# Kernel optimization log

Hardware: AMD Instinct MI355X
Metric: run time of the kernel (lower is better)

The kernel has to match this reference:

```python
import jax, jax.numpy as jnp
import numpy as np

EMBED_DIM = 1024
NUM_HEADS = 16
HEAD_DIM = EMBED_DIM // NUM_HEADS
CHUNK_SIZE = 10
LEFT_CONTEXT = 25
RIGHT_CONTEXT = 0
NEG_INF = -1e30  # stands in for float('-inf') additive mask, safe under softmax


def chunk_attention_mask(seq_len: int) -> jnp.ndarray:
    """Vectorized version of the per-row Python loop mask builder.
    Row i may attend to: its own chunk [chunk_start, chunk_end), the left
    context [i-left_context, chunk_start), and the right context
    [chunk_end, i+right_context+1)."""
    i = jnp.arange(seq_len)[:, None]
    j = jnp.arange(seq_len)[None, :]
    chunk_start = (i // CHUNK_SIZE) * CHUNK_SIZE
    chunk_end = jnp.minimum(chunk_start + CHUNK_SIZE, seq_len)
    in_chunk = (j >= chunk_start) & (j < chunk_end)
    in_left = (j >= i - LEFT_CONTEXT) & (j < chunk_start)
    in_right = (j >= chunk_end) & (j < jnp.minimum(seq_len, i + RIGHT_CONTEXT + 1))
    allowed = in_chunk | in_left | in_right
    return jnp.where(allowed, 0.0, NEG_INF).astype(jnp.float32)


def setup_inputs() -> dict:
    key = jax.random.key(0)
    ks = jax.random.split(key, 9)
    B, S, E = 2, 2048, EMBED_DIM
    s = 1.0 / np.sqrt(E)
    return {
        "hidden_states": jax.random.normal(ks[0], (B, S, E), jnp.float32),
        "Wq": jax.random.normal(ks[1], (E, E), jnp.float32) * s,
        "bq": jax.random.normal(ks[2], (E,), jnp.float32) * 0.02,
        "Wk": jax.random.normal(ks[3], (E, E), jnp.float32) * s,
        "bk": jax.random.normal(ks[4], (E,), jnp.float32) * 0.02,
        "Wv": jax.random.normal(ks[5], (E, E), jnp.float32) * s,
        "bv": jax.random.normal(ks[6], (E,), jnp.float32) * 0.02,
        "Wo": jax.random.normal(ks[7], (E, E), jnp.float32) * s,
        "bo": jax.random.normal(ks[8], (E,), jnp.float32) * 0.02,
    }


def reference(hidden_states, Wq, bq, Wk, bk, Wv, bv, Wo, bo):
    B, S, E = hidden_states.shape
    H, D = NUM_HEADS, HEAD_DIM
    scaling = D ** -0.5

    def proj(x, W, b):  # nn.Linear: x @ W.T + b, then split heads -> [B,H,S,D]
        y = jnp.einsum('bse,fe->bsf', x, W) + b
        return y.reshape(B, S, H, D).transpose(0, 2, 1, 3)

    q = proj(hidden_states, Wq, bq) * scaling
    k = proj(hidden_states, Wk, bk)
    v = proj(hidden_states, Wv, bv)

    scores = jnp.einsum('bhsd,bhtd->bhst', q, k)  # [B,H,S,S]
    scores = scores + chunk_attention_mask(S)[None, None]
    probs = jax.nn.softmax(scores, axis=-1)
    out = jnp.einsum('bhst,bhtd->bhsd', probs, v)  # [B,H,S,D]
    out = out.transpose(0, 2, 1, 3).reshape(B, S, E)
    out = jnp.einsum('bse,fe->bsf', out, Wo) + bo
    return out
```

## Files before the change

kernel.cpp:

```cpp
#include <hip/hip_runtime.h>
#include <stdint.h>

typedef unsigned short u16;
typedef __attribute__((ext_vector_type(8))) short short8;
typedef __attribute__((ext_vector_type(4))) short short4v;
typedef __attribute__((ext_vector_type(4))) float f32x4;

#define AS1 __attribute__((address_space(1)))
#define AS3 __attribute__((address_space(3)))

__device__ __forceinline__ u16 f2bf(float f) {
  uint32_t x = __builtin_bit_cast(uint32_t, f);
  uint32_t r = (x + 0x7fffu + ((x >> 16) & 1u)) >> 16;
  return (u16)r;
}
__device__ __forceinline__ float bf2f(u16 u) {
  return __builtin_bit_cast(float, (uint32_t)u << 16);
}

__device__ __forceinline__ void conv8(const float* __restrict__ s, u16* __restrict__ d, float sc) {
  float4 a = *(const float4*)s;
  float4 b = *(const float4*)(s + 4);
  union { u16 u[8]; uint4 v; } pk;
  pk.u[0] = f2bf(a.x * sc); pk.u[1] = f2bf(a.y * sc); pk.u[2] = f2bf(a.z * sc); pk.u[3] = f2bf(a.w * sc);
  pk.u[4] = f2bf(b.x * sc); pk.u[5] = f2bf(b.y * sc); pk.u[6] = f2bf(b.z * sc); pk.u[7] = f2bf(b.w * sc);
  *(uint4*)d = pk.v;
}
__device__ __forceinline__ void copy8f(const float* __restrict__ s, float* __restrict__ d, float sc) {
  float4 a = *(const float4*)s;
  float4 b = *(const float4*)(s + 4);
  a.x *= sc; a.y *= sc; a.z *= sc; a.w *= sc;
  b.x *= sc; b.y *= sc; b.z *= sc; b.w *= sc;
  *(float4*)d = a; *(float4*)(d + 4) = b;
}

__global__ void pack_kernel(const float* __restrict__ X,
                            const float* __restrict__ Wq, const float* __restrict__ bq,
                            const float* __restrict__ Wk, const float* __restrict__ bk,
                            const float* __restrict__ Wv, const float* __restrict__ bv,
                            const float* __restrict__ Wo,
                            u16* __restrict__ Xbf, u16* __restrict__ Wcat,
                            u16* __restrict__ Wobf, float* __restrict__ bcat) {
  int t = blockIdx.x * blockDim.x + threadIdx.x;
  if (t < 524288) { conv8(X + (size_t)t * 8, Xbf + (size_t)t * 8, 1.f); return; }
  t -= 524288;
  if (t < 131072) { conv8(Wq + (size_t)t * 8, Wcat + (size_t)t * 8, 0.125f); return; }
  t -= 131072;
  if (t < 131072) { conv8(Wk + (size_t)t * 8, Wcat + 1048576 + (size_t)t * 8, 1.f); return; }
  t -= 131072;
  if (t < 131072) { conv8(Wv + (size_t)t * 8, Wcat + 2097152 + (size_t)t * 8, 1.f); return; }
  t -= 131072;
  if (t < 131072) { conv8(Wo + (size_t)t * 8, Wobf + (size_t)t * 8, 1.f); return; }
  t -= 131072;
  if (t < 128) { copy8f(bq + t * 8, bcat + t * 8, 0.125f); return; }
  t -= 128;
  if (t < 128) { copy8f(bk + t * 8, bcat + 1024 + t * 8, 1.f); return; }
  t -= 128;
  if (t < 128) { copy8f(bv + t * 8, bcat + 2048 + t * 8, 1.f); return; }
}

template <int BN, bool OUT_BF16>
__global__ __launch_bounds__(256)
void gemm_bt(const u16* __restrict__ A, const u16* __restrict__ Bt,
             const float* __restrict__ bias, u16* __restrict__ Cbf,
             float* __restrict__ Cf, int M, int N, int K) {
  constexpr int SEG_A = 8;
  constexpr int SEG_B = BN / 16;
  constexpr int NSEG = SEG_A + SEG_B;
  constexpr int NI = BN / 32;
  __shared__ u16 As[2][128 * 32];
  __shared__ u16 Bs[2][BN * 32];
  const int wv = threadIdx.x >> 6;
  const int lane = threadIdx.x & 63;
  const int bm = blockIdx.x, bn = blockIdx.y;
  const int wm = wv >> 1, wn = wv & 1;
  const int lrow = lane & 15, quad = lane >> 4;

  f32x4 acc[4][NI];
#pragma unroll
  for (int i = 0; i < 4; ++i)
#pragma unroll
    for (int j = 0; j < NI; ++j) acc[i][j] = (f32x4){0.f, 0.f, 0.f, 0.f};

  const long arow = (long)bm * 128;
  const long brow = (long)bn * BN;
  const int srow = lane >> 2;
  const int scol = ((lane & 3) ^ ((lane >> 3) & 3)) * 8;
  const int swz = (quad ^ ((lrow >> 1) & 3)) * 8;

  auto stage = [&](int nb, int k0) {
#pragma unroll
    for (int it = 0; it < NSEG / 4; ++it) {
      const int s = wv * (NSEG / 4) + it;
      const u16* g;
      u16* l;
      if (s < SEG_A) {
        g = A + (arow + s * 16 + srow) * K + k0 + scol;
        l = (u16*)As[nb] + s * 512;
      } else {
        g = Bt + (brow + (s - SEG_A) * 16 + srow) * K + k0 + scol;
        l = (u16*)Bs[nb] + (s - SEG_A) * 512;
      }
      __builtin_amdgcn_global_load_lds((AS1 void*)g, (AS3 void*)l, 16, 0, 0);
    }
  };

  stage(0, 0);
  int cur = 0;
  for (int k0 = 0; k0 < K; k0 += 32) {
    __syncthreads();
    if (k0 + 32 < K) stage(cur ^ 1, k0 + 32);

    short8 af[4], bfr[NI];
#pragma unroll
    for (int mi = 0; mi < 4; ++mi)
      af[mi] = *(const short8*)(As[cur] + (wm * 64 + mi * 16 + lrow) * 32 + swz);
#pragma unroll
    for (int ni = 0; ni < NI; ++ni)
      bfr[ni] = *(const short8*)(Bs[cur] + (wn * (BN / 2) + ni * 16 + lrow) * 32 + swz);
#pragma unroll
    for (int mi = 0; mi < 4; ++mi)
#pragma unroll
      for (int ni = 0; ni < NI; ++ni)
        acc[mi][ni] = __builtin_amdgcn_mfma_f32_16x16x32_bf16(af[mi], bfr[ni], acc[mi][ni], 0, 0, 0);
    cur ^= 1;
  }

#pragma unroll
  for (int mi = 0; mi < 4; ++mi) {
#pragma unroll
    for (int ni = 0; ni < NI; ++ni) {
      const int col = bn * BN + wn * (BN / 2) + ni * 16 + lrow;
      const float bv = bias[col];
#pragma unroll
      for (int r = 0; r < 4; ++r) {
        const int row = bm * 128 + wm * 64 + mi * 16 + quad * 4 + r;
        const float v = acc[mi][ni][r] + bv;
        if constexpr (OUT_BF16) Cbf[(long)row * N + col] = f2bf(v);
        else Cf[(long)row * N + col] = v;
      }
    }
  }
}

#define NCH 205
#define VT_STRIDE 68
#define PB_STRIDE 72
#define WAVE_LDS (64 * VT_STRIDE + 16 * PB_STRIDE)

__global__ __launch_bounds__(256)
void attn_kernel(const u16* __restrict__ QKV, u16* __restrict__ ctx) {
  __shared__ __align__(16) u16 lds[4 * WAVE_LDS];
  const int wv = threadIdx.x >> 6;
  const int lane = threadIdx.x & 63;
  u16* Vt = lds + wv * WAVE_LDS;
  u16* Pb = Vt + 64 * VT_STRIDE;

  const int n = lane & 15, quad = lane >> 4;

  const int gw = blockIdx.x * 4 + wv;
  const int b = gw / (16 * NCH);
  int rem = gw - b * 16 * NCH;
  const int h = rem / NCH;
  const int c = rem - h * NCH;
  const int cs = c * 10;
  const int nq = min(10, 2048 - cs);
  const int w0 = max(cs - 25, 0);
  const int L = cs + nq - w0;

  const long base = ((long)b * 2048) * 3072 + (long)h * 64;

  for (int idx = lane; idx < (64 * VT_STRIDE) / 8; idx += 64)
    *(uint4*)(Vt + idx * 8) = (uint4){0, 0, 0, 0};
  for (int idx = lane; idx < (16 * PB_STRIDE) / 8; idx += 64)
    *(uint4*)(Pb + idx * 8) = (uint4){0, 0, 0, 0};

  for (int j = 0; j < L; ++j)
    Vt[lane * VT_STRIDE + j] = QKV[base + (long)(w0 + j) * 3072 + 2048 + lane];

  const int mclamp = min(n, nq - 1);
  const long qrow = base + (long)(cs + mclamp) * 3072;
  short8 aq0 = *(const short8*)(QKV + qrow + quad * 8);
  short8 aq1 = *(const short8*)(QKV + qrow + 32 + quad * 8);

  f32x4 sc[3];
#pragma unroll
  for (int t = 0; t < 3; ++t) {
    const int jj = min(16 * t + n, L - 1);
    const long krow = base + (long)(w0 + jj) * 3072 + 1024;
    short8 bk0 = *(const short8*)(QKV + krow + quad * 8);
    short8 bk1 = *(const short8*)(QKV + krow + 32 + quad * 8);
    f32x4 z = (f32x4){0.f, 0.f, 0.f, 0.f};
    z = __builtin_amdgcn_mfma_f32_16x16x32_bf16(aq0, bk0, z, 0, 0, 0);
    sc[t] = __builtin_amdgcn_mfma_f32_16x16x32_bf16(aq1, bk1, z, 0, 0, 0);
  }

#pragma unroll
  for (int r = 0; r < 4; ++r) {
    const int i = cs + quad * 4 + r;
    const int jlo = max(i - 25, 0) - w0;
    float v0 = (n >= jlo && n < L)      ? sc[0][r] : -1e30f;
    float v1 = (16 + n >= jlo && 16 + n < L) ? sc[1][r] : -1e30f;
    float v2 = (32 + n >= jlo && 32 + n < L) ? sc[2][r] : -1e30f;
    float m = fmaxf(v0, fmaxf(v1, v2));
#pragma unroll
    for (int off = 8; off > 0; off >>= 1) m = fmaxf(m, __shfl_xor(m, off));
    float p0 = __expf(v0 - m), p1 = __expf(v1 - m), p2 = __expf(v2 - m);
    float sum = p0 + p1 + p2;
#pragma unroll
    for (int off = 8; off > 0; off >>= 1) sum += __shfl_xor(sum, off);
    const float inv = 1.f / sum;
    u16* prow = Pb + (quad * 4 + r) * PB_STRIDE;
    prow[n]      = f2bf(p0 * inv);
    prow[16 + n] = f2bf(p1 * inv);
    prow[32 + n] = f2bf(p2 * inv);
  }

  short8 ap0 = *(const short8*)(Pb + n * PB_STRIDE + quad * 8);
  short8 ap1 = *(const short8*)(Pb + n * PB_STRIDE + 32 + quad * 8);
  f32x4 o[4];
#pragma unroll
  for (int dt = 0; dt < 4; ++dt) {
    const u16* vrow = Vt + (dt * 16 + n) * VT_STRIDE;
    short4v l0 = *(const short4v*)(vrow + quad * 8);
    short4v h0 = *(const short4v*)(vrow + quad * 8 + 4);
    short4v l1 = *(const short4v*)(vrow + 32 + quad * 8);
    short4v h1 = *(const short4v*)(vrow + 32 + quad * 8 + 4);
    short8 bv0 = __builtin_shufflevector(l0, h0, 0, 1, 2, 3, 4, 5, 6, 7);
    short8 bv1 = __builtin_shufflevector(l1, h1, 0, 1, 2, 3, 4, 5, 6, 7);
    f32x4 z = (f32x4){0.f, 0.f, 0.f, 0.f};
    z = __builtin_amdgcn_mfma_f32_16x16x32_bf16(ap0, bv0, z, 0, 0, 0);
    o[dt] = __builtin_amdgcn_mfma_f32_16x16x32_bf16(ap1, bv1, z, 0, 0, 0);
  }

#pragma unroll
  for (int dt = 0; dt < 4; ++dt) {
#pragma unroll
    for (int r = 0; r < 4; ++r) {
      const int row = quad * 4 + r;
      if (row < nq)
        ctx[((long)b * 2048 + cs + row) * 1024 + h * 64 + dt * 16 + n] = f2bf(o[dt][r]);
    }
  }
}

extern "C" void kernel_launch(void* const* d_in, const int* in_sizes, int n_in,
                              void* d_out, int out_size, void* d_ws, size_t ws_size,
                              hipStream_t stream) {
  const float* X  = (const float*)d_in[0];
  const float* Wq = (const float*)d_in[1];
  const float* bq = (const float*)d_in[2];
  const float* Wk = (const float*)d_in[3];
  const float* bk = (const float*)d_in[4];
  const float* Wv = (const float*)d_in[5];
  const float* bv = (const float*)d_in[6];
  const float* Wo = (const float*)d_in[7];
  const float* bo = (const float*)d_in[8];
  float* out = (float*)d_out;

  char* ws = (char*)d_ws;
  u16* Xbf   = (u16*)(ws);
  u16* Wcat  = (u16*)(ws + 8388608);
  u16* Wobf  = (u16*)(ws + 14680064);
  float* bcat = (float*)(ws + 16777216);
  u16* QKV   = (u16*)(ws + 16789504);
  u16* ctx   = (u16*)(ws + 41955328);

  pack_kernel<<<4098, 256, 0, stream>>>(X, Wq, bq, Wk, bk, Wv, bv, Wo, Xbf, Wcat, Wobf, bcat);
  gemm_bt<128, true ><<<dim3(32, 24), 256, 0, stream>>>(Xbf, Wcat, bcat, QKV, nullptr, 4096, 3072, 1024);
  attn_kernel<<<1640, 256, 0, stream>>>(QKV, ctx);
  gemm_bt<64, false><<<dim3(32, 16), 256, 0, stream>>>(ctx, Wobf, bo, nullptr, out, 4096, 1024, 1024);
}
```

Measured before the change: 163.0 us.

## Triple-buffer GEMM LDS stages with explicit vmcnt waits for deeper prefetch

Changes the bf16 GEMM mainloop from double to triple buffering in LDS, issuing global-to-LDS loads two k-steps ahead. Manual s_waitcnt vmcnt counts replace the implicit full wait, so a single barrier per iteration only waits for the oldest stage. The aim is to hide more global load latency. In exchange it uses more LDS per block, which may lower occupancy, and the hand-tuned vmcnt values depend on the per-wave load count.

```diff
diff --git a/kernel.cpp b/kernel.cpp
--- a/kernel.cpp
+++ b/kernel.cpp
@@ -67,9 +67,10 @@
   constexpr int SEG_A = 8;
   constexpr int SEG_B = BN / 16;
   constexpr int NSEG = SEG_A + SEG_B;
+  constexpr int LPW = NSEG / 4;
   constexpr int NI = BN / 32;
-  __shared__ u16 As[2][128 * 32];
-  __shared__ u16 Bs[2][BN * 32];
+  __shared__ u16 As[3][128 * 32];
+  __shared__ u16 Bs[3][BN * 32];
   const int wv = threadIdx.x >> 6;
   const int lane = threadIdx.x & 63;
   const int bm = blockIdx.x, bn = blockIdx.y;
@@ -90,8 +91,8 @@
 
   auto stage = [&](int nb, int k0) {
 #pragma unroll
-    for (int it = 0; it < NSEG / 4; ++it) {
-      const int s = wv * (NSEG / 4) + it;
+    for (int it = 0; it < LPW; ++it) {
+      const int s = wv * LPW + it;
       const u16* g;
       u16* l;
       if (s < SEG_A) {
@@ -105,25 +106,38 @@
     }
   };
 
+  const int T = K >> 5;
   stage(0, 0);
-  int cur = 0;
-  for (int k0 = 0; k0 < K; k0 += 32) {
-    __syncthreads();
-    if (k0 + 32 < K) stage(cur ^ 1, k0 + 32);
-
+  stage(1, 32);
+  int cb = 0;
+  for (int i = 0; i < T; ++i) {
+    if (i < T - 1) {
+      if constexpr (LPW == 4) asm volatile("s_waitcnt vmcnt(4)" ::: "memory");
+      else                    asm volatile("s_waitcnt vmcnt(3)" ::: "memory");
+    } else {
+      asm volatile("s_waitcnt vmcnt(0)" ::: "memory");
+    }
+    __builtin_amdgcn_s_barrier();
+    if (i + 2 < T) {
+      const int sb = (cb + 2 >= 3) ? cb - 1 : cb + 2;
+      stage(sb, (i + 2) * 32);
+    }
+
+    const u16* Ab = As[cb];
+    const u16* Bb = Bs[cb];
     short8 af[4], bfr[NI];
 #pragma unroll
     for (int mi = 0; mi < 4; ++mi)
-      af[mi] = *(const short8*)(As[cur] + (wm * 64 + mi * 16 + lrow) * 32 + swz);
+      af[mi] = *(const short8*)(Ab + (wm * 64 + mi * 16 + lrow) * 32 + swz);
 #pragma unroll
     for (int ni = 0; ni < NI; ++ni)
-      bfr[ni] = *(const short8*)(Bs[cur] + (wn * (BN / 2) + ni * 16 + lrow) * 32 + swz);
+      bfr[ni] = *(const short8*)(Bb + (wn * (BN / 2) + ni * 16 + lrow) * 32 + swz);
 #pragma unroll
     for (int mi = 0; mi < 4; ++mi)
 #pragma unroll
       for (int ni = 0; ni < NI; ++ni)
         acc[mi][ni] = __builtin_amdgcn_mfma_f32_16x16x32_bf16(af[mi], bfr[ni], acc[mi][ni], 0, 0, 0);
-    cur ^= 1;
+    cb = (cb == 2) ? 0 : cb + 1;
   }
 
 #pragma unroll
```

Result: no change. 166.1 us (+1.9%).
